# Kernel optimization log

Measured on AMD Instinct MI355X. Metric: run time of the kernel, lower is better.

Reference implementation:

```python
import jax, jax.numpy as jnp
import numpy as np

B, N, C = 8, 4096, 512
H = W = 64           # N = H * W, dimensionality == 2
SHIFT = 4            # shift_size
WS = 8               # window_size
R = 4                # mlp_ratio
EPS = 1e-6


def setup_inputs() -> dict:
    key = jax.random.key(0)
    ks = jax.random.split(key, 3)
    return {
        "inputs": jax.random.normal(ks[0], (B, N, C), dtype=jnp.float32),
        # second_norm (LayerNormalization) params
        "ln_gamma": jnp.ones((C,), jnp.float32),
        "ln_beta": jnp.zeros((C,), jnp.float32),
        # MLP params: Dense(C*R) -> gelu -> Dense(C)
        "W1": jax.random.normal(ks[1], (C, C * R), dtype=jnp.float32) * 0.02,
        "b1": jnp.zeros((C * R,), jnp.float32),
        "W2": jax.random.normal(ks[2], (C * R, C), dtype=jnp.float32) * 0.02,
        "b2": jnp.zeros((C,), jnp.float32),
    }


def _layer_norm(x, gamma, beta):
    mu = jnp.mean(x, axis=-1, keepdims=True)
    var = jnp.mean(jnp.square(x - mu), axis=-1, keepdims=True)
    return (x - mu) * jax.lax.rsqrt(var + EPS) * gamma + beta


def reference(inputs, ln_gamma, ln_beta, W1, b1, W2, b2):
    # NOTE: faithful to the provided call(): first_norm and attention are
    # never invoked (`normed = x`, `self_att = windowed`), so the window
    # partition + reverse is an exact identity round-trip of the shifted grid.
    grid = inputs.reshape(B, H, W, C)
    shifted = jnp.roll(grid, (-SHIFT, -SHIFT), axis=(1, 2))  # SwinCyclicShifter

    # window partition: [B, nH, nW, WS, WS, C] windows of WSxWS patches
    nh = H // WS
    win = shifted.reshape(B, nh, WS, nh, WS, C).transpose(0, 1, 3, 2, 4, 5)
    # (identity "attention" on [B*nH*nW, WS*WS, C]) then window reverse
    unwin = win.transpose(0, 1, 3, 2, 4, 5).reshape(B, N, C)

    x = unwin + inputs                       # residual add
    normed = _layer_norm(x, ln_gamma, ln_beta)
    h = jax.nn.gelu(normed @ W1 + b1)        # [B, N, 4C]
    mlp_out = h @ W2 + b2                    # [B, N, C]
    return mlp_out + x
```

## Files before the change

### kernel.cpp

```cpp
#include <hip/hip_runtime.h>
#include <hip/hip_bf16.h>
#include <cstdint>
#include <cstddef>


typedef short bf16x8 __attribute__((ext_vector_type(8)));
typedef float f32x4 __attribute__((ext_vector_type(4)));

#define GLOBAL_AS(p) ((__attribute__((address_space(1))) void*)(uintptr_t)(p))
#define LDS_AS(p)    ((__attribute__((address_space(3))) void*)(p))

static __device__ __forceinline__ ushort f2bf(float f) {
    uint32_t u = __float_as_uint(f);
    uint32_t r = (u + 0x7FFFu + ((u >> 16) & 1u)) >> 16;
    return (ushort)r;
}

static __device__ __forceinline__ float gelu_s(float v) {
    float v2 = v * v;
    float m = fmaf(0.07135481283f, v2, 1.5957691216f);
    float e = __expf(-v * m);
    return v * __builtin_amdgcn_rcpf(1.0f + e);
}

static __device__ __forceinline__ int rolled_row(int row) {
    int b = row >> 12, n = row & 4095;
    int h = n >> 6, wv = n & 63;
    int n2 = (((h + 4) & 63) << 6) | ((wv + 4) & 63);
    return (b << 12) | n2;
}

#define SBAR() do { __builtin_amdgcn_sched_barrier(0); \
                    __builtin_amdgcn_s_barrier(); \
                    __builtin_amdgcn_sched_barrier(0); } while (0)

__global__ __launch_bounds__(128)
void ln_kernel(const float* __restrict__ in, const float* __restrict__ gamma,
               const float* __restrict__ beta, ushort* __restrict__ normed) {
    const int row = blockIdx.x;
    const int t = threadIdx.x;
    const int row2 = rolled_row(row);

    const float4* p0 = (const float4*)(in + (size_t)row * 512);
    const float4* p1 = (const float4*)(in + (size_t)row2 * 512);
    float4 a = p0[t], c = p1[t];
    float x0 = a.x + c.x, x1 = a.y + c.y, x2 = a.z + c.z, x3 = a.w + c.w;

    float s = x0 + x1 + x2 + x3;
    float sq = x0 * x0 + x1 * x1 + x2 * x2 + x3 * x3;
#pragma unroll
    for (int o = 32; o > 0; o >>= 1) {
        s += __shfl_xor(s, o);
        sq += __shfl_xor(sq, o);
    }
    __shared__ float red[4];
    if ((t & 63) == 0) { red[(t >> 6) * 2] = s; red[(t >> 6) * 2 + 1] = sq; }
    __syncthreads();
    s = red[0] + red[2];
    sq = red[1] + red[3];
    float mu = s * (1.0f / 512.0f);
    float var = sq * (1.0f / 512.0f) - mu * mu;
    float rs = rsqrtf(var + 1e-6f);

    float4 g = ((const float4*)gamma)[t];
    float4 be = ((const float4*)beta)[t];
    ushort4 o4;
    o4.x = f2bf((x0 - mu) * rs * g.x + be.x);
    o4.y = f2bf((x1 - mu) * rs * g.y + be.y);
    o4.z = f2bf((x2 - mu) * rs * g.z + be.z);
    o4.w = f2bf((x3 - mu) * rs * g.w + be.w);
    ((ushort4*)(normed + (size_t)row * 512))[t] = o4;
}

template <int PERM>
__global__ __launch_bounds__(256)
void transpose_cast(const float* __restrict__ src, ushort* __restrict__ dst,
                    int R, int Ccols) {
    __shared__ float tile[32][33];
    const int bx = blockIdx.x * 32;
    const int by = blockIdx.y * 32;
    const int tx = threadIdx.x, ty = threadIdx.y;
#pragma unroll
    for (int i = 0; i < 32; i += 8)
        tile[ty + i][tx] = src[(size_t)(by + ty + i) * Ccols + bx + tx];
    __syncthreads();
    int k = by + tx;
    int kd = PERM ? ((k & ~63) | ((k & 15) << 2) | ((k >> 4) & 3)) : k;
#pragma unroll
    for (int i = 0; i < 32; i += 8)
        dst[(size_t)(bx + ty + i) * R + kd] = f2bf(tile[tx][ty + i]);
}

__global__ __launch_bounds__(256)
void mlp_gemm1(const ushort* __restrict__ A, const ushort* __restrict__ Bt,
               const float* __restrict__ bias, ushort* __restrict__ outH) {
    constexpr int K = 512, N = 2048, BK = 64;
    __shared__ ushort Asm[128 * BK];
    __shared__ ushort Bsm[128 * BK];

    const int t = threadIdx.x;
    const int w = t >> 6, l = t & 63;
    const int wr = w >> 1, wc = w & 1;

    const int bid = blockIdx.x;
    const int xcd = bid & 7, idx = bid >> 3;
    const int brow = ((xcd << 5) + (idx >> 4)) << 7;
    const int bcol = (idx & 15) << 7;

    f32x4 acc[4][4] = {};

    const int trow = t >> 3;
    const int csrc = (((t & 7) ^ ((t >> 3) & 7)) << 3);
    const size_t aBase = (size_t)(brow + trow) * K + csrc;
    const size_t bBase = (size_t)(bcol + trow) * K + csrc;
    char* const ldsA = (char*)Asm + w * 1024;
    char* const ldsB = (char*)Bsm + w * 1024;

    const int rA = l & 15;
    const int cbase = ((l >> 4) ^ (rA & 7)) << 4;
    const int preA = (wr << 13) + (rA << 7) + cbase;
    const int preB = (wc << 13) + (rA << 7) + cbase;

    for (int k0 = 0; k0 < K; k0 += BK) {
#pragma unroll
        for (int i = 0; i < 4; ++i) {
            __builtin_amdgcn_global_load_lds(GLOBAL_AS(A + aBase + (size_t)(i * 32) * K + k0),
                                             LDS_AS(ldsA + i * 4096), 16, 0, 0);
            __builtin_amdgcn_global_load_lds(GLOBAL_AS(Bt + bBase + (size_t)(i * 32) * K + k0),
                                             LDS_AS(ldsB + i * 4096), 16, 0, 0);
        }
        __syncthreads();

#pragma unroll
        for (int s = 0; s < 2; ++s) {
            const int so = s << 6;
            bf16x8 aF[4], bF[4];
#pragma unroll
            for (int i = 0; i < 4; ++i)
                aF[i] = *(const bf16x8*)((const char*)Asm + ((preA + i * 2048) ^ so));
#pragma unroll
            for (int j = 0; j < 4; ++j)
                bF[j] = *(const bf16x8*)((const char*)Bsm + ((preB + j * 2048) ^ so));
#pragma unroll
            for (int i = 0; i < 4; ++i)
#pragma unroll
                for (int j = 0; j < 4; ++j)
                    acc[i][j] = __builtin_amdgcn_mfma_f32_16x16x32_bf16(aF[i], bF[j], acc[i][j], 0, 0, 0);
        }
        __syncthreads();
    }

    const int cm = (l >> 4) << 2;
    const int cn = l & 15;
    float bvv[4];
#pragma unroll
    for (int j = 0; j < 4; ++j)
        bvv[j] = bias[bcol + wc * 64 + j * 16 + cn];
    const int ecol = bcol + wc * 64 + (cn << 2);
#pragma unroll
    for (int i = 0; i < 4; ++i) {
#pragma unroll
        for (int r = 0; r < 4; ++r) {
            const int row = brow + wr * 64 + i * 16 + cm + r;
            float f0 = gelu_s(acc[i][0][r] + bvv[0]);
            float f1 = gelu_s(acc[i][1][r] + bvv[1]);
            float f2 = gelu_s(acc[i][2][r] + bvv[2]);
            float f3 = gelu_s(acc[i][3][r] + bvv[3]);
            uint32_t lo, hi;
            asm("v_cvt_pk_bf16_f32 %0, %1, %2" : "=v"(lo) : "v"(f0), "v"(f1));
            asm("v_cvt_pk_bf16_f32 %0, %1, %2" : "=v"(hi) : "v"(f2), "v"(f3));
            uint2 pv; pv.x = lo; pv.y = hi;
            *(uint2*)(outH + (size_t)row * N + ecol) = pv;
        }
    }
}

__global__ __launch_bounds__(512, 2)
void mlp_gemm2(const ushort* __restrict__ A, const ushort* __restrict__ Bt,
               const float* __restrict__ bias, const float* __restrict__ resid,
               float* __restrict__ outF) {
    constexpr int KT = 2048, TT = 32, N = 512;
    __shared__ __align__(16) char sm[131072];
    const int t = threadIdx.x;
    const int w = t >> 6, l = t & 63;
    const int wr = w >> 2, wc = w & 3;

    const int nwg = gridDim.x;
    const int bid = blockIdx.x;
    const int swz = (bid & 7) * (nwg >> 3) + (bid >> 3);
    const int cb = swz & 1;
    const int rgrp = swz >> 1;
    const int brow0 = rgrp * 256;
    const int bcol = cb << 8;

    const int kksw = (((t & 3) ^ ((t >> 4) & 3)) << 3);
    const size_t aTh = (size_t)(t >> 2) * KT + kksw;
    const size_t bTh = (size_t)(bcol + (t >> 2)) * KT + kksw;
    const ushort* const aPanel = A + (size_t)brow0 * KT;
    char* const dA = (char*)sm + (w << 10);
    char* const dB = dA + 65536;

    const int xorv = ((l >> 2) & 3) << 4;
    const int preA = ((((wr << 7) + (l & 15)) << 6) + ((l >> 4) << 4)) ^ xorv;
    const int preB = 65536 + (((((wc << 6) + (l & 15)) << 6) + ((l >> 4) << 4)) ^ xorv);

    f32x4 acc[8][4] = {};
    bf16x8 aF[4], bF[4];

    auto issueA = [&](int T, int kh) {
        const int slot = ((T & 1) << 1) | kh;
        const ushort* s = aPanel + aTh + T * 64 + kh * 32;
        char* d = dA + (slot << 14);
        __builtin_amdgcn_global_load_lds(GLOBAL_AS(s), LDS_AS(d), 16, 0, 0);
        __builtin_amdgcn_global_load_lds(GLOBAL_AS(s + (size_t)128 * KT), LDS_AS(d + 8192), 16, 0, 0);
    };
    auto issueB = [&](int T, int kh) {
        const int slot = ((T & 1) << 1) | kh;
        const ushort* s = Bt + bTh + T * 64 + kh * 32;
        char* d = dB + (slot << 14);
        __builtin_amdgcn_global_load_lds(GLOBAL_AS(s), LDS_AS(d), 16, 0, 0);
        __builtin_amdgcn_global_load_lds(GLOBAL_AS(s + (size_t)128 * KT), LDS_AS(d + 8192), 16, 0, 0);
    };
    auto rdA = [&](int slot, int mb) {
        const char* p = (const char*)sm + (slot << 14) + preA + (mb << 12);
        aF[0] = *(const bf16x8*)(p);
        aF[1] = *(const bf16x8*)(p + 1024);
        aF[2] = *(const bf16x8*)(p + 2048);
        aF[3] = *(const bf16x8*)(p + 3072);
    };
    auto rdB = [&](int slot) {
        const char* p = (const char*)sm + (slot << 14) + preB;
        bF[0] = *(const bf16x8*)(p);
        bF[1] = *(const bf16x8*)(p + 1024);
        bF[2] = *(const bf16x8*)(p + 2048);
        bF[3] = *(const bf16x8*)(p + 3072);
    };
    auto mfma16 = [&](int mb) {
        __builtin_amdgcn_s_setprio(1);
#pragma unroll
        for (int mf = 0; mf < 4; ++mf)
#pragma unroll
            for (int nf = 0; nf < 4; ++nf)
                acc[mb * 4 + mf][nf] = __builtin_amdgcn_mfma_f32_16x16x32_bf16(
                    aF[mf], bF[nf], acc[mb * 4 + mf][nf], 0, 0, 0);
        __builtin_amdgcn_s_setprio(0);
    };

    issueA(0, 0); issueB(0, 0);
    issueA(0, 1); issueB(0, 1);
    issueA(1, 0); issueB(1, 0);
    issueA(1, 1);
    __builtin_amdgcn_sched_barrier(0);
    asm volatile("s_waitcnt vmcnt(6)" ::: "memory");
    SBAR();

#pragma unroll 1
    for (int T = 0; T < TT; ++T) {
        const int s0 = (T & 1) << 1;
        rdA(s0, 0); rdB(s0);
        SBAR();
        if (T + 1 < TT) issueB(T + 1, 1);
        mfma16(0);
        SBAR();
        rdA(s0, 1);
        SBAR();
        if (T + 2 < TT) issueA(T + 2, 0);
        mfma16(1);
        SBAR();
        rdA(s0 + 1, 0); rdB(s0 + 1);
        SBAR();
        if (T + 2 < TT) issueB(T + 2, 0);
        mfma16(0);
        SBAR();
        rdA(s0 + 1, 1);
        SBAR();
        if (T + 2 < TT) issueA(T + 2, 1);
        mfma16(1);
        __builtin_amdgcn_sched_barrier(0);
        if (T < TT - 2)       { asm volatile("s_waitcnt vmcnt(6)" ::: "memory"); }
        else if (T == TT - 2) { asm volatile("s_waitcnt vmcnt(0)" ::: "memory"); }
        SBAR();
    }

#pragma unroll
    for (int h2 = 0; h2 < 2; ++h2) {
        if (wr == h2) {
#pragma unroll
            for (int mf = 0; mf < 8; ++mf)
#pragma unroll
                for (int nf = 0; nf < 4; ++nf)
#pragma unroll
                    for (int r = 0; r < 4; ++r) {
                        int rl = mf * 16 + ((l >> 4) << 2) + r;
                        int col = (wc << 6) + nf * 16 + (l & 15);
                        *(float*)(sm + rl * 1024 + col * 4) = acc[mf][nf][r];
                    }
        }
        __syncthreads();
#pragma unroll
        for (int k = 0; k < 16; ++k) {
            int c = t + (k << 9);
            int row = c >> 6, c4 = c & 63;
            f32x4 v = *(const f32x4*)(sm + ((size_t)c << 4));
            int R = brow0 + (h2 << 7) + row;
            int col0 = bcol + (c4 << 2);
            f32x4 bb = *(const f32x4*)(bias + col0);
            f32x4 x0 = *(const f32x4*)(resid + (size_t)R * 512 + col0);
            f32x4 x1 = *(const f32x4*)(resid + (size_t)rolled_row(R) * 512 + col0);
            v = v + bb + x0 + x1;
            *(f32x4*)(outF + (size_t)R * N + col0) = v;
        }
        __syncthreads();
    }
}

extern "C" void kernel_launch(void* const* d_in, const int* in_sizes, int n_in,
                              void* d_out, int out_size, void* d_ws, size_t ws_size,
                              hipStream_t stream) {
    const float* in = (const float*)d_in[0];
    const float* ln_g = (const float*)d_in[1];
    const float* ln_b = (const float*)d_in[2];
    const float* W1 = (const float*)d_in[3];
    const float* b1 = (const float*)d_in[4];
    const float* W2 = (const float*)d_in[5];
    const float* b2 = (const float*)d_in[6];
    float* out = (float*)d_out;

    char* ws = (char*)d_ws;
    ushort* normed = (ushort*)ws;
    ushort* hbuf   = (ushort*)(ws + (size_t)32 * 1024 * 1024);
    ushort* W1T    = (ushort*)(ws + (size_t)160 * 1024 * 1024);
    ushort* W2T    = (ushort*)(ws + (size_t)162 * 1024 * 1024);

    const int M = 32768;
    const int C = 512, C4 = 2048;

    ln_kernel<<<M, 128, 0, stream>>>(in, ln_g, ln_b, normed);
    transpose_cast<0><<<dim3(C4 / 32, C / 32), dim3(32, 8), 0, stream>>>(W1, W1T, C, C4);
    transpose_cast<1><<<dim3(C / 32, C4 / 32), dim3(32, 8), 0, stream>>>(W2, W2T, C4, C);

    mlp_gemm1<<<dim3(4096), 256, 0, stream>>>(normed, W1T, b1, hbuf);
    mlp_gemm2<<<dim3(256), 512, 0, stream>>>(hbuf, W2T, b2, in, out);
}
```

Baseline: 213.2 us.

## Store residual sum in bf16 from LN and prefetch it in GEMM2 epilogue

The layernorm kernel now also writes the residual sum x (input plus rolled input) as bf16 into a workspace buffer. The second GEMM prefetches that buffer into registers before its last k-tile, hiding the load latency, and adds it in the epilogue in place of reading two fp32 rows, one of them a scattered rolled row. This halves the epilogue residual traffic, but adds a 32MB write in the LN kernel, many extra registers in GEMM2, and bf16 rounding on the residual path. The new path runs only when the workspace holds at least 196MB.

```diff
diff --git a/kernel.cpp b/kernel.cpp
--- a/kernel.cpp
+++ b/kernel.cpp
@@ -34,9 +34,11 @@
                     __builtin_amdgcn_s_barrier(); \
                     __builtin_amdgcn_sched_barrier(0); } while (0)
 
+template <int XS>
 __global__ __launch_bounds__(128)
 void ln_kernel(const float* __restrict__ in, const float* __restrict__ gamma,
-               const float* __restrict__ beta, ushort* __restrict__ normed) {
+               const float* __restrict__ beta, ushort* __restrict__ normed,
+               ushort* __restrict__ xsum) {
     const int row = blockIdx.x;
     const int t = threadIdx.x;
     const int row2 = rolled_row(row);
@@ -45,6 +47,12 @@
     const float4* p1 = (const float4*)(in + (size_t)row2 * 512);
     float4 a = p0[t], c = p1[t];
     float x0 = a.x + c.x, x1 = a.y + c.y, x2 = a.z + c.z, x3 = a.w + c.w;
+
+    if constexpr (XS) {
+        ushort4 xo;
+        xo.x = f2bf(x0); xo.y = f2bf(x1); xo.z = f2bf(x2); xo.w = f2bf(x3);
+        ((ushort4*)(xsum + (size_t)row * 512))[t] = xo;
+    }
 
     float s = x0 + x1 + x2 + x3;
     float sq = x0 * x0 + x1 * x1 + x2 * x2 + x3 * x3;
@@ -175,10 +183,11 @@
     }
 }
 
+template <int XS>
 __global__ __launch_bounds__(512, 2)
 void mlp_gemm2(const ushort* __restrict__ A, const ushort* __restrict__ Bt,
                const float* __restrict__ bias, const float* __restrict__ resid,
-               float* __restrict__ outF) {
+               const ushort* __restrict__ xsum, float* __restrict__ outF) {
     constexpr int KT = 2048, TT = 32, N = 512;
     __shared__ __align__(16) char sm[131072];
     const int t = threadIdx.x;
@@ -246,6 +255,33 @@
         __builtin_amdgcn_s_setprio(0);
     };
 
+    auto tile_body = [&](int T) {
+        const int s0 = (T & 1) << 1;
+        rdA(s0, 0); rdB(s0);
+        SBAR();
+        if (T + 1 < TT) issueB(T + 1, 1);
+        mfma16(0);
+        SBAR();
+        rdA(s0, 1);
+        SBAR();
+        if (T + 2 < TT) issueA(T + 2, 0);
+        mfma16(1);
+        SBAR();
+        rdA(s0 + 1, 0); rdB(s0 + 1);
+        SBAR();
+        if (T + 2 < TT) issueB(T + 2, 0);
+        mfma16(0);
+        SBAR();
+        rdA(s0 + 1, 1);
+        SBAR();
+        if (T + 2 < TT) issueA(T + 2, 1);
+        mfma16(1);
+        __builtin_amdgcn_sched_barrier(0);
+        if (T < TT - 2)       { asm volatile("s_waitcnt vmcnt(6)" ::: "memory"); }
+        else if (T == TT - 2) { asm volatile("s_waitcnt vmcnt(0)" ::: "memory"); }
+        SBAR();
+    };
+
     issueA(0, 0); issueB(0, 0);
     issueA(0, 1); issueB(0, 1);
     issueA(1, 0); issueB(1, 0);
@@ -255,32 +291,22 @@
     SBAR();
 
 #pragma unroll 1
-    for (int T = 0; T < TT; ++T) {
-        const int s0 = (T & 1) << 1;
-        rdA(s0, 0); rdB(s0);
-        SBAR();
-        if (T + 1 < TT) issueB(T + 1, 1);
-        mfma16(0);
-        SBAR();
-        rdA(s0, 1);
-        SBAR();
-        if (T + 2 < TT) issueA(T + 2, 0);
-        mfma16(1);
-        SBAR();
-        rdA(s0 + 1, 0); rdB(s0 + 1);
-        SBAR();
-        if (T + 2 < TT) issueB(T + 2, 0);
-        mfma16(0);
-        SBAR();
-        rdA(s0 + 1, 1);
-        SBAR();
-        if (T + 2 < TT) issueA(T + 2, 1);
-        mfma16(1);
-        __builtin_amdgcn_sched_barrier(0);
-        if (T < TT - 2)       { asm volatile("s_waitcnt vmcnt(6)" ::: "memory"); }
-        else if (T == TT - 2) { asm volatile("s_waitcnt vmcnt(0)" ::: "memory"); }
-        SBAR();
-    }
+    for (int T = 0; T < TT - 1; ++T)
+        tile_body(T);
+
+    uint2 xsA[16], xsB[16];
+    if constexpr (XS) {
+#pragma unroll
+        for (int k = 0; k < 16; ++k) {
+            int c = t + (k << 9);
+            int R0 = brow0 + (c >> 6);
+            size_t off = (size_t)R0 * 512 + bcol + ((c & 63) << 2);
+            xsA[k] = *(const uint2*)(xsum + off);
+            xsB[k] = *(const uint2*)(xsum + off + (size_t)128 * 512);
+        }
+    }
+
+    tile_body(TT - 1);
 
 #pragma unroll
     for (int h2 = 0; h2 < 2; ++h2) {
@@ -305,9 +331,19 @@
             int R = brow0 + (h2 << 7) + row;
             int col0 = bcol + (c4 << 2);
             f32x4 bb = *(const f32x4*)(bias + col0);
-            f32x4 x0 = *(const f32x4*)(resid + (size_t)R * 512 + col0);
-            f32x4 x1 = *(const f32x4*)(resid + (size_t)rolled_row(R) * 512 + col0);
-            v = v + bb + x0 + x1;
+            if constexpr (XS) {
+                uint2 xv = h2 ? xsB[k] : xsA[k];
+                f32x4 xf;
+                xf[0] = __uint_as_float(xv.x << 16);
+                xf[1] = __uint_as_float(xv.x & 0xffff0000u);
+                xf[2] = __uint_as_float(xv.y << 16);
+                xf[3] = __uint_as_float(xv.y & 0xffff0000u);
+                v = v + bb + xf;
+            } else {
+                f32x4 x0 = *(const f32x4*)(resid + (size_t)R * 512 + col0);
+                f32x4 x1 = *(const f32x4*)(resid + (size_t)rolled_row(R) * 512 + col0);
+                v = v + bb + x0 + x1;
+            }
             *(f32x4*)(outF + (size_t)R * N + col0) = v;
         }
         __syncthreads();
@@ -331,14 +367,23 @@
     ushort* hbuf   = (ushort*)(ws + (size_t)32 * 1024 * 1024);
     ushort* W1T    = (ushort*)(ws + (size_t)160 * 1024 * 1024);
     ushort* W2T    = (ushort*)(ws + (size_t)162 * 1024 * 1024);
+    ushort* xsum   = (ushort*)(ws + (size_t)164 * 1024 * 1024);
+    const bool xs = ws_size >= (size_t)196 * 1024 * 1024;
 
     const int M = 32768;
     const int C = 512, C4 = 2048;
 
-    ln_kernel<<<M, 128, 0, stream>>>(in, ln_g, ln_b, normed);
+    if (xs)
+        ln_kernel<1><<<M, 128, 0, stream>>>(in, ln_g, ln_b, normed, xsum);
+    else
+        ln_kernel<0><<<M, 128, 0, stream>>>(in, ln_g, ln_b, normed, nullptr);
     transpose_cast<0><<<dim3(C4 / 32, C / 32), dim3(32, 8), 0, stream>>>(W1, W1T, C, C4);
     transpose_cast<1><<<dim3(C / 32, C4 / 32), dim3(32, 8), 0, stream>>>(W2, W2T, C4, C);
 
     mlp_gemm1<<<dim3(4096), 256, 0, stream>>>(normed, W1T, b1, hbuf);
-    mlp_gemm2<<<dim3(256), 512, 0, stream>>>(hbuf, W2T, b2, in, out);
-}
+
+    if (xs)
+        mlp_gemm2<1><<<dim3(256), 512, 0, stream>>>(hbuf, W2T, b2, in, xsum, out);
+    else
+        mlp_gemm2<0><<<dim3(256), 512, 0, stream>>>(hbuf, W2T, b2, in, nullptr, out);
+}
```

Measured after the change: 249.7 us. +17.1%, slower.
